# Kernel optimization log

Measured on AMD Instinct MI355X. Metric: run time of the kernel, lower is better.

## Reference

```python
import jax, jax.numpy as jnp
import numpy as np

KNN_K = 3
EPS = 1e-8


def _make_poses(key, batch):
    """Random valid SE(3) matrices [B,4,4] (rotation via QR, small translation)."""
    k1, k2 = jax.random.split(key)
    A = jax.random.normal(k1, (batch, 3, 3), dtype=jnp.float32)
    Q, _ = jnp.linalg.qr(A)
    det = jnp.linalg.det(Q)[:, None, None]
    Q = Q * jnp.where(det < 0, -1.0, 1.0)  # ensure proper rotation
    t = jax.random.normal(k2, (batch, 3), dtype=jnp.float32) * 0.5
    pose = jnp.tile(jnp.eye(4, dtype=jnp.float32), (batch, 1, 1))
    pose = pose.at[:, :3, :3].set(Q)
    pose = pose.at[:, :3, 3].set(t)
    return pose


def setup_inputs() -> dict:
    key = jax.random.key(0)
    kq, kr, kf, kp0, kp1 = jax.random.split(key, 5)
    B, N, M = 2, 8192, 8192
    pc0 = jax.random.normal(kq, (B, N, 3), dtype=jnp.float32) * 20.0
    pc1 = jax.random.normal(kr, (B, M, 3), dtype=jnp.float32) * 20.0
    flow1 = jax.random.normal(kf, (B, M, 3), dtype=jnp.float32)
    pose0 = _make_poses(kp0, B)
    pose1 = _make_poses(kp1, B)
    return {"pc0": pc0, "pc1": pc1, "flow1": flow1, "pose0": pose0, "pose1": pose1}


def reference(pc0, pc1, flow1, pose0, pose1):
    # cal_pose0to1: transform from pc0 ego frame into pc1 ego frame
    pose_0to1 = jnp.linalg.inv(pose1) @ pose0            # [B,4,4]
    R = pose_0to1[:, :3, :3]                             # [B,3,3]
    t = pose_0to1[:, :3, 3]                              # [B,3]
    # pc0_in_pc1 = pc0 @ R^T + t
    pc0_t = jnp.einsum("bij,bnj->bni", R, pc0) + t[:, None, :]  # [B,N,3]
    pose_flow = pc0_t - pc0                              # ego-motion displacement

    # pairwise squared distances (cdist^2) via GEMM form: [B,N,M]
    q2 = jnp.sum(pc0_t * pc0_t, axis=-1)                 # [B,N]
    r2 = jnp.sum(pc1 * pc1, axis=-1)                     # [B,M]
    cross = jnp.einsum("bnd,bmd->bnm", pc0_t, pc1)
    d2 = q2[:, :, None] + r2[:, None, :] - 2.0 * cross

    # KNN: k smallest distances
    neg_d2, idx = jax.lax.top_k(-d2, KNN_K)              # [B,N,k]
    d = jnp.sqrt(jnp.maximum(-neg_d2, 0.0))

    # inverse-distance weights over the k neighbors
    w = 1.0 / (d + EPS)
    w = w / jnp.sum(w, axis=-1, keepdims=True)           # [B,N,k]

    # gather neighbor flows: flow1 [B,M,3] -> [B,N,k,3]
    gathered = jnp.take_along_axis(flow1[:, None, :, :], idx[..., None], axis=2)
    flow_interp = jnp.sum(w[..., None] * gathered, axis=2)  # [B,N,3]
    return flow_interp, pose_flow
```

## Files before the change

### kernel.cpp

```cpp
#include <hip/hip_runtime.h>
#include <math.h>
#include <float.h>
#include <limits.h>

#define CS   64
#define CT   32
#define TILE_PTS (CT * CS)
#define CSP  65
#define QB1  64
#define QT   16
#define MARGIN 0.05f
typedef unsigned long long ull;
typedef float v2f __attribute__((ext_vector_type(2)));
#define KMAX 0xFFFFFFFFFFFFFFFFull

__device__ __forceinline__ unsigned int ford(float f) {
    unsigned int b = __float_as_uint(f);
    return b ^ (((unsigned int)((int)b >> 31)) | 0x80000000u);
}
__device__ __forceinline__ float funord(unsigned int u) {
    unsigned int m = ((u >> 31) - 1u) | 0x80000000u;
    return __uint_as_float(u ^ m);
}

__device__ __forceinline__ ull umin64(ull a, ull b) { return a < b ? a : b; }
__device__ __forceinline__ ull umax64(ull a, ull b) { return a > b ? a : b; }

__device__ __forceinline__ void ins3k(ull k, ull& k0, ull& k1, ull& k2) {
    ull n2 = umax64(k1, umin64(k2, k));
    ull n1 = umax64(k0, umin64(k1, k));
    k0 = umin64(k0, k);
    k1 = n1;
    k2 = n2;
}

__device__ __forceinline__ void sins(float d, float& a0, float& a1, float& a2)
{
    float n1 = __builtin_amdgcn_fmed3f(a0, a1, d);
    float n2 = __builtin_amdgcn_fmed3f(a1, a2, d);
    a0 = fminf(a0, d);
    a1 = n1;
    a2 = n2;
}

__device__ __forceinline__ void pose_rel(const float* __restrict__ P0,
                                         const float* __restrict__ P1,
                                         float R[3][3], float tv[3])
{
    float dt0 = P0[3]  - P1[3];
    float dt1 = P0[7]  - P1[7];
    float dt2 = P0[11] - P1[11];
    #pragma unroll
    for (int i = 0; i < 3; ++i) {
        float a0 = P1[i], a1 = P1[4 + i], a2 = P1[8 + i];
        #pragma unroll
        for (int j = 0; j < 3; ++j)
            R[i][j] = fmaf(a2, P0[8 + j], fmaf(a1, P0[4 + j], a0 * P0[j]));
        tv[i] = fmaf(a2, dt2, fmaf(a1, dt1, a0 * dt0));
    }
}

__launch_bounds__(256, 3)
__global__ void knn_phaseA(const float* __restrict__ pc0,
                           const float* __restrict__ pc1,
                           const float* __restrict__ pose0,
                           const float* __restrict__ pose1,
                           float* __restrict__ cmin,
                           int B, int N, int M, int cstride)
{
    __shared__ float4 tile[CT * CSP];
    __shared__ float4 qd[QB1];

    const int tid = threadIdx.x;
    const int b   = blockIdx.z;
    const int ctb = blockIdx.y;
    const int qb  = blockIdx.x * QB1;
    const int pbase = ctb * TILE_PTS;

    if (tid < QB1) {
        float R[3][3], tv[3];
        pose_rel(pose0 + b * 16, pose1 + b * 16, R, tv);
        int qg0 = qb + tid;
        int qg  = (qg0 < N) ? qg0 : (N - 1);
        const float px = pc0[(size_t)(b * N + qg) * 3 + 0];
        const float py = pc0[(size_t)(b * N + qg) * 3 + 1];
        const float pz = pc0[(size_t)(b * N + qg) * 3 + 2];
        float qx = fmaf(R[0][2], pz, fmaf(R[0][1], py, R[0][0] * px)) + tv[0];
        float qy = fmaf(R[1][2], pz, fmaf(R[1][1], py, R[1][0] * px)) + tv[1];
        float qz = fmaf(R[2][2], pz, fmaf(R[2][1], py, R[2][0] * px)) + tv[2];
        qd[tid] = make_float4(qx, qy, qz,
                              (qx * qx + qy * qy) + qz * qz);
    }

    #pragma unroll
    for (int k = 0; k < TILE_PTS / (256 * 4); ++k) {
        const int pl = (tid + k * 256) * 4;
        const int p  = pbase + pl;
        const int c  = pl >> 6;
        const int off = pl & (CS - 1);
        float4* dst = &tile[c * CSP + off];
        float x0,y0,z0, x1,y1,z1, x2,y2,z2, x3,y3,z3;
        if (p + 3 < M) {
            const float4* pf = (const float4*)(pc1 + (size_t)(b * M + p) * 3);
            float4 A = pf[0], Bv = pf[1], C = pf[2];
            x0 = A.x;  y0 = A.y;  z0 = A.z;
            x1 = A.w;  y1 = Bv.x; z1 = Bv.y;
            x2 = Bv.z; y2 = Bv.w; z2 = C.x;
            x3 = C.y;  y3 = C.z;  z3 = C.w;
        } else {
            float tx[4], ty[4], tz[4];
            #pragma unroll
            for (int u = 0; u < 4; ++u) {
                int pp = p + u;
                if (pp < M) {
                    const float* s = pc1 + (size_t)(b * M + pp) * 3;
                    tx[u] = s[0]; ty[u] = s[1]; tz[u] = s[2];
                } else {
                    tx[u] = 0.f; ty[u] = 0.f; tz[u] = 0.f;
                }
            }
            x0 = tx[0]; y0 = ty[0]; z0 = tz[0];
            x1 = tx[1]; y1 = ty[1]; z1 = tz[1];
            x2 = tx[2]; y2 = ty[2]; z2 = tz[2];
            x3 = tx[3]; y3 = ty[3]; z3 = tz[3];
        }
        float r0 = (p + 0 < M) ? (x0 * x0 + y0 * y0) + z0 * z0 : FLT_MAX;
        float r1 = (p + 1 < M) ? (x1 * x1 + y1 * y1) + z1 * z1 : FLT_MAX;
        float r2 = (p + 2 < M) ? (x2 * x2 + y2 * y2) + z2 * z2 : FLT_MAX;
        float r3 = (p + 3 < M) ? (x3 * x3 + y3 * y3) + z3 * z3 : FLT_MAX;
        dst[0] = make_float4(-2.f * x0, -2.f * x1, -2.f * y0, -2.f * y1);
        dst[1] = make_float4(-2.f * z0, -2.f * z1, r0, r1);
        dst[2] = make_float4(-2.f * x2, -2.f * x3, -2.f * y2, -2.f * y3);
        dst[3] = make_float4(-2.f * z2, -2.f * z3, r2, r3);
    }
    __syncthreads();

    const int w    = tid >> 6;
    const int lane = tid & 63;
    const int cl   = lane & 31;
    const int part = lane >> 5;

    v2f qx2[QT], qy2[QT], qz2[QT];
    #pragma unroll
    for (int t = 0; t < QT; ++t) {
        float4 qq = qd[w * QT + t];
        qx2[t] = (v2f)(qq.x);
        qy2[t] = (v2f)(qq.y);
        qz2[t] = (v2f)(qq.z);
    }

    float mm[QT];
    #pragma unroll
    for (int t = 0; t < QT; ++t) mm[t] = FLT_MAX;

    const float4* tp = &tile[cl * CSP + part * 32];
    #pragma unroll 2
    for (int i2 = 0; i2 < 16; ++i2) {
        const float4 xy = tp[2 * i2];
        const float4 zw = tp[2 * i2 + 1];
        v2f X = {xy.x, xy.y};
        v2f Y = {xy.z, xy.w};
        v2f Z = {zw.x, zw.y};
        v2f W = {zw.z, zw.w};
        #pragma unroll
        for (int t = 0; t < QT; ++t) {
            v2f kk;
            asm("v_pk_fma_f32 %0, %1, %2, %3"
                : "=v"(kk) : "v"(Z), "v"(qz2[t]), "v"(W));
            asm("v_pk_fma_f32 %0, %1, %2, %0"
                : "+v"(kk) : "v"(Y), "v"(qy2[t]));
            asm("v_pk_fma_f32 %0, %1, %2, %0"
                : "+v"(kk) : "v"(X), "v"(qx2[t]));
            mm[t] = fminf(mm[t], fminf(kk.x, kk.y));
        }
    }

    #pragma unroll
    for (int t = 0; t < QT; ++t)
        mm[t] = fminf(mm[t], __shfl_xor(mm[t], 32));

    if (part == 0) {
        const int cg = ctb * CT + cl;
        #pragma unroll
        for (int t = 0; t < QT; ++t) {
            int qg0 = qb + w * QT + t;
            int qg  = (qg0 < N) ? qg0 : (N - 1);
            cmin[((size_t)b * N + qg) * cstride + cg] = mm[t];
        }
    }
}

__launch_bounds__(256, 8)
__global__ void knn_select(const float* __restrict__ pc0,
                           const float* __restrict__ pc1,
                           const float* __restrict__ flow1,
                           const float* __restrict__ pose0,
                           const float* __restrict__ pose1,
                           const float* __restrict__ cmin,
                           float* __restrict__ out,
                           int B, int N, int M, int cstride)
{
    const int tid  = threadIdx.x;
    const int w    = tid >> 6;
    const int lane = tid & 63;
    const int g    = lane >> 4;
    const int l    = lane & 15;

    const int bx = blockIdx.x;
    int qbi, sub;
    if ((gridDim.x & 31) == 0) {
        qbi = (bx & 7) + 8 * (bx >> 5);
        sub = (bx >> 3) & 3;
    } else {
        qbi = bx >> 2;
        sub = bx & 3;
    }

    const int b    = blockIdx.y;
    const int q0   = qbi * QB1 + sub * 16 + w * 4 + g;
    const bool qvalid = (q0 < N);
    const int q    = qvalid ? q0 : (N - 1);

    const size_t row = (size_t)(b * N + q) * cstride;
    const float4 sA = *(const float4*)&cmin[row + l * 8];
    const float4 sB = *(const float4*)&cmin[row + l * 8 + 4];

    float R[3][3], tv[3];
    pose_rel(pose0 + b * 16, pose1 + b * 16, R, tv);
    const float px = pc0[(size_t)(b * N + q) * 3 + 0];
    const float py = pc0[(size_t)(b * N + q) * 3 + 1];
    const float pz = pc0[(size_t)(b * N + q) * 3 + 2];
    const float qx = fmaf(R[0][2], pz, fmaf(R[0][1], py, R[0][0] * px)) + tv[0];
    const float qy = fmaf(R[1][2], pz, fmaf(R[1][1], py, R[1][0] * px)) + tv[1];
    const float qz = fmaf(R[2][2], pz, fmaf(R[2][1], py, R[2][0] * px)) + tv[2];
    const float q2 = (qx * qx + qy * qy) + qz * qz;

    float a0 = FLT_MAX, a1 = FLT_MAX, a2 = FLT_MAX;
    sins(sA.x, a0, a1, a2); sins(sA.y, a0, a1, a2);
    sins(sA.z, a0, a1, a2); sins(sA.w, a0, a1, a2);
    sins(sB.x, a0, a1, a2); sins(sB.y, a0, a1, a2);
    sins(sB.z, a0, a1, a2); sins(sB.w, a0, a1, a2);
    #pragma unroll
    for (int msk = 1; msk <= 8; msk <<= 1) {
        float o0 = __shfl_xor(a0, msk);
        float o1 = __shfl_xor(a1, msk);
        float o2 = __shfl_xor(a2, msk);
        sins(o0, a0, a1, a2);
        sins(o1, a0, a1, a2);
        sins(o2, a0, a1, a2);
    }
    const float thr = a2 + MARGIN;

    unsigned int mbits =
          ((unsigned int)(sA.x <= thr) << 0) | ((unsigned int)(sA.y <= thr) << 1)
        | ((unsigned int)(sA.z <= thr) << 2) | ((unsigned int)(sA.w <= thr) << 3)
        | ((unsigned int)(sB.x <= thr) << 4) | ((unsigned int)(sB.y <= thr) << 5)
        | ((unsigned int)(sB.z <= thr) << 6) | ((unsigned int)(sB.w <= thr) << 7);
    ull m0 = (l < 8) ? ((ull)mbits << (8 * l)) : 0ull;
    ull m1 = (l >= 8) ? ((ull)mbits << (8 * (l - 8))) : 0ull;
    #pragma unroll
    for (int msk = 1; msk <= 8; msk <<= 1) {
        m0 |= __shfl_xor(m0, msk);
        m1 |= __shfl_xor(m1, msk);
    }

    ull kA0 = KMAX, kA1 = KMAX, kA2 = KMAX;
    ull kB0 = KMAX, kB1 = KMAX, kB2 = KMAX;
    #pragma unroll
    for (int half = 0; half < 2; ++half) {
        ull mask = half ? m1 : m0;
        const int cbase = half * 64;
        while (mask) {
            const int ck = (int)__builtin_ctzll(mask);
            mask &= mask - 1;
            const int mb = (cbase + ck) * CS;
            #pragma unroll
            for (int r = 0; r < CS / 16; ++r) {
                const int m = mb + r * 16 + l;
                if (m < M) {
                    const float* pp = pc1 + (size_t)(b * M + m) * 3;
                    float x = pp[0], y = pp[1], z = pp[2];
                    float r2 = (x * x + y * y) + z * z;
                    float cr = fmaf(qz, z, fmaf(qy, y, qx * x));
                    float dd = fmaf(-2.0f, cr, q2 + r2);
                    ull kk = ((ull)ford(dd) << 32) | (unsigned int)m;
                    if (r & 1) ins3k(kk, kB0, kB1, kB2);
                    else       ins3k(kk, kA0, kA1, kA2);
                }
            }
        }
    }
    ins3k(kB0, kA0, kA1, kA2);
    ins3k(kB1, kA0, kA1, kA2);
    ins3k(kB2, kA0, kA1, kA2);

    #pragma unroll
    for (int msk = 1; msk <= 8; msk <<= 1) {
        ull o0 = __shfl_xor(kA0, msk);
        ull o1 = __shfl_xor(kA1, msk);
        ull o2 = __shfl_xor(kA2, msk);
        ins3k(o0, kA0, kA1, kA2);
        ins3k(o1, kA0, kA1, kA2);
        ins3k(o2, kA0, kA1, kA2);
    }

    if (l == 0 && qvalid) {
        size_t pf = (size_t)B * N * 3 + (size_t)(b * N + q) * 3;
        out[pf + 0] = qx - px;
        out[pf + 1] = qy - py;
        out[pf + 2] = qz - pz;

        float D0 = funord((unsigned int)(kA0 >> 32));
        float D1 = funord((unsigned int)(kA1 >> 32));
        float D2 = funord((unsigned int)(kA2 >> 32));
        int   i0 = (int)(unsigned int)kA0;
        int   i1 = (int)(unsigned int)kA1;
        int   i2 = (int)(unsigned int)kA2;

        float dd0 = sqrtf(fmaxf(D0, 0.f));
        float dd1 = sqrtf(fmaxf(D1, 0.f));
        float dd2 = sqrtf(fmaxf(D2, 0.f));
        float w0 = 1.0f / (dd0 + 1e-8f);
        float w1 = 1.0f / (dd1 + 1e-8f);
        float w2 = 1.0f / (dd2 + 1e-8f);
        float wsum = (w0 + w1) + w2;
        w0 /= wsum; w1 /= wsum; w2 /= wsum;

        const float* f0 = flow1 + (size_t)(b * M + i0) * 3;
        const float* f1 = flow1 + (size_t)(b * M + i1) * 3;
        const float* f2 = flow1 + (size_t)(b * M + i2) * 3;

        const size_t ob = (size_t)(b * N + q) * 3;
        #pragma unroll
        for (int c = 0; c < 3; ++c) {
            float p0 = w0 * f0[c];
            float p1 = w1 * f1[c];
            float p2 = w2 * f2[c];
            out[ob + c] = (p0 + p1) + p2;
        }
    }
}

extern "C" void kernel_launch(void* const* d_in, const int* in_sizes, int n_in,
                              void* d_out, int out_size, void* d_ws, size_t ws_size,
                              hipStream_t stream) {
    const float* pc0   = (const float*)d_in[0];
    const float* pc1   = (const float*)d_in[1];
    const float* flow1 = (const float*)d_in[2];
    const float* pose0 = (const float*)d_in[3];
    const float* pose1 = (const float*)d_in[4];
    float* out = (float*)d_out;

    const int B = in_sizes[3] / 16;
    const int N = in_sizes[0] / (3 * B);
    const int M = in_sizes[1] / (3 * B);

    const int nct     = (M + TILE_PTS - 1) / TILE_PTS;
    const int cstride = nct * CT;

    float* cmin = (float*)d_ws;

    dim3 g1((N + QB1 - 1) / QB1, nct, B);
    knn_phaseA<<<g1, dim3(256), 0, stream>>>(pc0, pc1, pose0, pose1,
                                             cmin, B, N, M, cstride);

    dim3 g2((N + 15) / 16, B);
    knn_select<<<g2, dim3(256), 0, stream>>>(pc0, pc1, flow1, pose0, pose1,
                                             cmin, out, B, N, M, cstride);
}
```

Before: 35.66 us.

## Fuse chunk-min distance pass and KNN selection into one kernel

Merges the two-kernel KNN pipeline into a single kernel. Each 512-thread block scans all reference points for its 64 queries in two LDS-tiled passes and keeps the per-chunk minima in shared memory instead of global workspace. It then runs the threshold-and-rescan selection and the flow interpolation in place. This removes the global cmin write and read and one kernel launch, but the grid shrinks to one block per query group, which lowers parallelism. The pass count and cmin stride are hardcoded to cover M up to 8192.

```diff
diff --git a/kernel.cpp b/kernel.cpp
--- a/kernel.cpp
+++ b/kernel.cpp
@@ -3,12 +3,14 @@
 #include <float.h>
 #include <limits.h>
 
-#define CS   64
-#define CT   32
-#define TILE_PTS (CT * CS)
-#define CSP  65
-#define QB1  64
-#define QT   16
+#define CS    64
+#define CTP   64
+#define PASS_PTS (CTP * CS)
+#define CSP   65
+#define QPB   64
+#define QT    8
+#define NPASS 2
+#define CMSTRIDE 132
 #define MARGIN 0.05f
 typedef unsigned long long ull;
 typedef float v2f __attribute__((ext_vector_type(2)));
@@ -60,85 +62,46 @@
     }
 }
 
-__launch_bounds__(256, 3)
-__global__ void knn_phaseA(const float* __restrict__ pc0,
-                           const float* __restrict__ pc1,
-                           const float* __restrict__ pose0,
-                           const float* __restrict__ pose1,
-                           float* __restrict__ cmin,
-                           int B, int N, int M, int cstride)
+__launch_bounds__(512, 2)
+__global__ void knn_fused(const float* __restrict__ pc0,
+                          const float* __restrict__ pc1,
+                          const float* __restrict__ flow1,
+                          const float* __restrict__ pose0,
+                          const float* __restrict__ pose1,
+                          float* __restrict__ out,
+                          int B, int N, int M)
 {
-    __shared__ float4 tile[CT * CSP];
-    __shared__ float4 qd[QB1];
+    __shared__ float4 tile[CTP * CSP];
+    __shared__ float4 qd[QPB];
 
     const int tid = threadIdx.x;
-    const int b   = blockIdx.z;
-    const int ctb = blockIdx.y;
-    const int qb  = blockIdx.x * QB1;
-    const int pbase = ctb * TILE_PTS;
-
-    if (tid < QB1) {
+    const int b   = blockIdx.y;
+    const int qb  = blockIdx.x * QPB;
+
+    if (tid < QPB) {
         float R[3][3], tv[3];
         pose_rel(pose0 + b * 16, pose1 + b * 16, R, tv);
         int qg0 = qb + tid;
-        int qg  = (qg0 < N) ? qg0 : (N - 1);
+        bool valid = qg0 < N;
+        int qg = valid ? qg0 : (N - 1);
         const float px = pc0[(size_t)(b * N + qg) * 3 + 0];
         const float py = pc0[(size_t)(b * N + qg) * 3 + 1];
         const float pz = pc0[(size_t)(b * N + qg) * 3 + 2];
         float qx = fmaf(R[0][2], pz, fmaf(R[0][1], py, R[0][0] * px)) + tv[0];
         float qy = fmaf(R[1][2], pz, fmaf(R[1][1], py, R[1][0] * px)) + tv[1];
         float qz = fmaf(R[2][2], pz, fmaf(R[2][1], py, R[2][0] * px)) + tv[2];
-        qd[tid] = make_float4(qx, qy, qz,
-                              (qx * qx + qy * qy) + qz * qz);
-    }
-
-    #pragma unroll
-    for (int k = 0; k < TILE_PTS / (256 * 4); ++k) {
-        const int pl = (tid + k * 256) * 4;
-        const int p  = pbase + pl;
-        const int c  = pl >> 6;
-        const int off = pl & (CS - 1);
-        float4* dst = &tile[c * CSP + off];
-        float x0,y0,z0, x1,y1,z1, x2,y2,z2, x3,y3,z3;
-        if (p + 3 < M) {
-            const float4* pf = (const float4*)(pc1 + (size_t)(b * M + p) * 3);
-            float4 A = pf[0], Bv = pf[1], C = pf[2];
-            x0 = A.x;  y0 = A.y;  z0 = A.z;
-            x1 = A.w;  y1 = Bv.x; z1 = Bv.y;
-            x2 = Bv.z; y2 = Bv.w; z2 = C.x;
-            x3 = C.y;  y3 = C.z;  z3 = C.w;
-        } else {
-            float tx[4], ty[4], tz[4];
-            #pragma unroll
-            for (int u = 0; u < 4; ++u) {
-                int pp = p + u;
-                if (pp < M) {
-                    const float* s = pc1 + (size_t)(b * M + pp) * 3;
-                    tx[u] = s[0]; ty[u] = s[1]; tz[u] = s[2];
-                } else {
-                    tx[u] = 0.f; ty[u] = 0.f; tz[u] = 0.f;
-                }
-            }
-            x0 = tx[0]; y0 = ty[0]; z0 = tz[0];
-            x1 = tx[1]; y1 = ty[1]; z1 = tz[1];
-            x2 = tx[2]; y2 = ty[2]; z2 = tz[2];
-            x3 = tx[3]; y3 = ty[3]; z3 = tz[3];
-        }
-        float r0 = (p + 0 < M) ? (x0 * x0 + y0 * y0) + z0 * z0 : FLT_MAX;
-        float r1 = (p + 1 < M) ? (x1 * x1 + y1 * y1) + z1 * z1 : FLT_MAX;
-        float r2 = (p + 2 < M) ? (x2 * x2 + y2 * y2) + z2 * z2 : FLT_MAX;
-        float r3 = (p + 3 < M) ? (x3 * x3 + y3 * y3) + z3 * z3 : FLT_MAX;
-        dst[0] = make_float4(-2.f * x0, -2.f * x1, -2.f * y0, -2.f * y1);
-        dst[1] = make_float4(-2.f * z0, -2.f * z1, r0, r1);
-        dst[2] = make_float4(-2.f * x2, -2.f * x3, -2.f * y2, -2.f * y3);
-        dst[3] = make_float4(-2.f * z2, -2.f * z3, r2, r3);
+        qd[tid] = make_float4(qx, qy, qz, (qx * qx + qy * qy) + qz * qz);
+        if (valid) {
+            size_t pf = (size_t)B * N * 3 + (size_t)(b * N + qg) * 3;
+            out[pf + 0] = qx - px;
+            out[pf + 1] = qy - py;
+            out[pf + 2] = qz - pz;
+        }
     }
     __syncthreads();
 
     const int w    = tid >> 6;
     const int lane = tid & 63;
-    const int cl   = lane & 31;
-    const int part = lane >> 5;
 
     v2f qx2[QT], qy2[QT], qz2[QT];
     #pragma unroll
@@ -149,194 +112,204 @@
         qz2[t] = (v2f)(qq.z);
     }
 
-    float mm[QT];
+    float mm[NPASS][QT];
     #pragma unroll
-    for (int t = 0; t < QT; ++t) mm[t] = FLT_MAX;
-
-    const float4* tp = &tile[cl * CSP + part * 32];
-    #pragma unroll 2
-    for (int i2 = 0; i2 < 16; ++i2) {
-        const float4 xy = tp[2 * i2];
-        const float4 zw = tp[2 * i2 + 1];
-        v2f X = {xy.x, xy.y};
-        v2f Y = {xy.z, xy.w};
-        v2f Z = {zw.x, zw.y};
-        v2f W = {zw.z, zw.w};
-        #pragma unroll
-        for (int t = 0; t < QT; ++t) {
-            v2f kk;
-            asm("v_pk_fma_f32 %0, %1, %2, %3"
-                : "=v"(kk) : "v"(Z), "v"(qz2[t]), "v"(W));
-            asm("v_pk_fma_f32 %0, %1, %2, %0"
-                : "+v"(kk) : "v"(Y), "v"(qy2[t]));
-            asm("v_pk_fma_f32 %0, %1, %2, %0"
-                : "+v"(kk) : "v"(X), "v"(qx2[t]));
-            mm[t] = fminf(mm[t], fminf(kk.x, kk.y));
-        }
-    }
-
+    for (int pp = 0; pp < NPASS; ++pp)
+        #pragma unroll
+        for (int t = 0; t < QT; ++t) mm[pp][t] = FLT_MAX;
+
+    for (int pass = 0; pass < NPASS; ++pass) {
+        if (pass) __syncthreads();
+
+        #pragma unroll
+        for (int k = 0; k < PASS_PTS / (512 * 4); ++k) {
+            const int pl = (tid + k * 512) * 4;
+            const int p  = pass * PASS_PTS + pl;
+            const int c  = pl >> 6;
+            const int off = pl & (CS - 1);
+            float4* dst = &tile[c * CSP + off];
+            float x0,y0,z0, x1,y1,z1, x2,y2,z2, x3,y3,z3;
+            if (p + 3 < M) {
+                const float4* pf = (const float4*)(pc1 + (size_t)(b * M + p) * 3);
+                float4 A = pf[0], Bv = pf[1], C = pf[2];
+                x0 = A.x;  y0 = A.y;  z0 = A.z;
+                x1 = A.w;  y1 = Bv.x; z1 = Bv.y;
+                x2 = Bv.z; y2 = Bv.w; z2 = C.x;
+                x3 = C.y;  y3 = C.z;  z3 = C.w;
+            } else {
+                float tx[4], ty[4], tz[4];
+                #pragma unroll
+                for (int u = 0; u < 4; ++u) {
+                    int pp2 = p + u;
+                    if (pp2 < M) {
+                        const float* s = pc1 + (size_t)(b * M + pp2) * 3;
+                        tx[u] = s[0]; ty[u] = s[1]; tz[u] = s[2];
+                    } else {
+                        tx[u] = 0.f; ty[u] = 0.f; tz[u] = 0.f;
+                    }
+                }
+                x0 = tx[0]; y0 = ty[0]; z0 = tz[0];
+                x1 = tx[1]; y1 = ty[1]; z1 = tz[1];
+                x2 = tx[2]; y2 = ty[2]; z2 = tz[2];
+                x3 = tx[3]; y3 = ty[3]; z3 = tz[3];
+            }
+            float r0 = (p + 0 < M) ? (x0 * x0 + y0 * y0) + z0 * z0 : FLT_MAX;
+            float r1 = (p + 1 < M) ? (x1 * x1 + y1 * y1) + z1 * z1 : FLT_MAX;
+            float r2 = (p + 2 < M) ? (x2 * x2 + y2 * y2) + z2 * z2 : FLT_MAX;
+            float r3 = (p + 3 < M) ? (x3 * x3 + y3 * y3) + z3 * z3 : FLT_MAX;
+            dst[0] = make_float4(-2.f * x0, -2.f * x1, -2.f * y0, -2.f * y1);
+            dst[1] = make_float4(-2.f * z0, -2.f * z1, r0, r1);
+            dst[2] = make_float4(-2.f * x2, -2.f * x3, -2.f * y2, -2.f * y3);
+            dst[3] = make_float4(-2.f * z2, -2.f * z3, r2, r3);
+        }
+        __syncthreads();
+
+        const float4* tp = &tile[lane * CSP];
+        #pragma unroll 4
+        for (int i = 0; i < 32; ++i) {
+            const float4 xy = tp[2 * i];
+            const float4 zw = tp[2 * i + 1];
+            v2f X = {xy.x, xy.y};
+            v2f Y = {xy.z, xy.w};
+            v2f Z = {zw.x, zw.y};
+            v2f W = {zw.z, zw.w};
+            #pragma unroll
+            for (int t = 0; t < QT; ++t) {
+                v2f kk;
+                asm("v_pk_fma_f32 %0, %1, %2, %3"
+                    : "=v"(kk) : "v"(Z), "v"(qz2[t]), "v"(W));
+                asm("v_pk_fma_f32 %0, %1, %2, %0"
+                    : "+v"(kk) : "v"(Y), "v"(qy2[t]));
+                asm("v_pk_fma_f32 %0, %1, %2, %0"
+                    : "+v"(kk) : "v"(X), "v"(qx2[t]));
+                mm[pass][t] = fminf(mm[pass][t], fminf(kk.x, kk.y));
+            }
+        }
+    }
+
+    __syncthreads();
+
+    float* cminL = (float*)tile;
     #pragma unroll
-    for (int t = 0; t < QT; ++t)
-        mm[t] = fminf(mm[t], __shfl_xor(mm[t], 32));
-
-    if (part == 0) {
-        const int cg = ctb * CT + cl;
-        #pragma unroll
-        for (int t = 0; t < QT; ++t) {
-            int qg0 = qb + w * QT + t;
-            int qg  = (qg0 < N) ? qg0 : (N - 1);
-            cmin[((size_t)b * N + qg) * cstride + cg] = mm[t];
-        }
-    }
-}
-
-__launch_bounds__(256, 8)
-__global__ void knn_select(const float* __restrict__ pc0,
-                           const float* __restrict__ pc1,
-                           const float* __restrict__ flow1,
-                           const float* __restrict__ pose0,
-                           const float* __restrict__ pose1,
-                           const float* __restrict__ cmin,
-                           float* __restrict__ out,
-                           int B, int N, int M, int cstride)
-{
-    const int tid  = threadIdx.x;
-    const int w    = tid >> 6;
-    const int lane = tid & 63;
-    const int g    = lane >> 4;
-    const int l    = lane & 15;
-
-    const int bx = blockIdx.x;
-    int qbi, sub;
-    if ((gridDim.x & 31) == 0) {
-        qbi = (bx & 7) + 8 * (bx >> 5);
-        sub = (bx >> 3) & 3;
-    } else {
-        qbi = bx >> 2;
-        sub = bx & 3;
-    }
-
-    const int b    = blockIdx.y;
-    const int q0   = qbi * QB1 + sub * 16 + w * 4 + g;
-    const bool qvalid = (q0 < N);
-    const int q    = qvalid ? q0 : (N - 1);
-
-    const size_t row = (size_t)(b * N + q) * cstride;
-    const float4 sA = *(const float4*)&cmin[row + l * 8];
-    const float4 sB = *(const float4*)&cmin[row + l * 8 + 4];
-
-    float R[3][3], tv[3];
-    pose_rel(pose0 + b * 16, pose1 + b * 16, R, tv);
-    const float px = pc0[(size_t)(b * N + q) * 3 + 0];
-    const float py = pc0[(size_t)(b * N + q) * 3 + 1];
-    const float pz = pc0[(size_t)(b * N + q) * 3 + 2];
-    const float qx = fmaf(R[0][2], pz, fmaf(R[0][1], py, R[0][0] * px)) + tv[0];
-    const float qy = fmaf(R[1][2], pz, fmaf(R[1][1], py, R[1][0] * px)) + tv[1];
-    const float qz = fmaf(R[2][2], pz, fmaf(R[2][1], py, R[2][0] * px)) + tv[2];
-    const float q2 = (qx * qx + qy * qy) + qz * qz;
-
-    float a0 = FLT_MAX, a1 = FLT_MAX, a2 = FLT_MAX;
-    sins(sA.x, a0, a1, a2); sins(sA.y, a0, a1, a2);
-    sins(sA.z, a0, a1, a2); sins(sA.w, a0, a1, a2);
-    sins(sB.x, a0, a1, a2); sins(sB.y, a0, a1, a2);
-    sins(sB.z, a0, a1, a2); sins(sB.w, a0, a1, a2);
-    #pragma unroll
-    for (int msk = 1; msk <= 8; msk <<= 1) {
-        float o0 = __shfl_xor(a0, msk);
-        float o1 = __shfl_xor(a1, msk);
-        float o2 = __shfl_xor(a2, msk);
-        sins(o0, a0, a1, a2);
-        sins(o1, a0, a1, a2);
-        sins(o2, a0, a1, a2);
-    }
-    const float thr = a2 + MARGIN;
-
-    unsigned int mbits =
-          ((unsigned int)(sA.x <= thr) << 0) | ((unsigned int)(sA.y <= thr) << 1)
-        | ((unsigned int)(sA.z <= thr) << 2) | ((unsigned int)(sA.w <= thr) << 3)
-        | ((unsigned int)(sB.x <= thr) << 4) | ((unsigned int)(sB.y <= thr) << 5)
-        | ((unsigned int)(sB.z <= thr) << 6) | ((unsigned int)(sB.w <= thr) << 7);
-    ull m0 = (l < 8) ? ((ull)mbits << (8 * l)) : 0ull;
-    ull m1 = (l >= 8) ? ((ull)mbits << (8 * (l - 8))) : 0ull;
-    #pragma unroll
-    for (int msk = 1; msk <= 8; msk <<= 1) {
-        m0 |= __shfl_xor(m0, msk);
-        m1 |= __shfl_xor(m1, msk);
-    }
-
-    ull kA0 = KMAX, kA1 = KMAX, kA2 = KMAX;
-    ull kB0 = KMAX, kB1 = KMAX, kB2 = KMAX;
-    #pragma unroll
-    for (int half = 0; half < 2; ++half) {
-        ull mask = half ? m1 : m0;
-        const int cbase = half * 64;
-        while (mask) {
-            const int ck = (int)__builtin_ctzll(mask);
-            mask &= mask - 1;
-            const int mb = (cbase + ck) * CS;
-            #pragma unroll
-            for (int r = 0; r < CS / 16; ++r) {
-                const int m = mb + r * 16 + l;
-                if (m < M) {
-                    const float* pp = pc1 + (size_t)(b * M + m) * 3;
-                    float x = pp[0], y = pp[1], z = pp[2];
-                    float r2 = (x * x + y * y) + z * z;
-                    float cr = fmaf(qz, z, fmaf(qy, y, qx * x));
-                    float dd = fmaf(-2.0f, cr, q2 + r2);
-                    ull kk = ((ull)ford(dd) << 32) | (unsigned int)m;
-                    if (r & 1) ins3k(kk, kB0, kB1, kB2);
-                    else       ins3k(kk, kA0, kA1, kA2);
+    for (int t = 0; t < QT; ++t) {
+        const int ql = w * QT + t;
+        cminL[ql * CMSTRIDE + lane]       = mm[0][t];
+        cminL[ql * CMSTRIDE + CTP + lane] = mm[1][t];
+    }
+    __syncthreads();
+
+    const int g = tid >> 4;
+    const int l = tid & 15;
+
+    for (int round = 0; round < QPB / 32; ++round) {
+        const int ql = round * 32 + g;
+        const int q0 = qb + ql;
+        const bool qvalid = (q0 < N);
+        const int q = qvalid ? q0 : (N - 1);
+
+        const float4 sA = *(const float4*)&cminL[ql * CMSTRIDE + l * 8];
+        const float4 sB = *(const float4*)&cminL[ql * CMSTRIDE + l * 8 + 4];
+        const float4 qq = qd[ql];
+        const float qx = qq.x, qy = qq.y, qz = qq.z, q2 = qq.w;
+
+        float a0 = FLT_MAX, a1 = FLT_MAX, a2 = FLT_MAX;
+        sins(sA.x, a0, a1, a2); sins(sA.y, a0, a1, a2);
+        sins(sA.z, a0, a1, a2); sins(sA.w, a0, a1, a2);
+        sins(sB.x, a0, a1, a2); sins(sB.y, a0, a1, a2);
+        sins(sB.z, a0, a1, a2); sins(sB.w, a0, a1, a2);
+        #pragma unroll
+        for (int msk = 1; msk <= 8; msk <<= 1) {
+            float o0 = __shfl_xor(a0, msk);
+            float o1 = __shfl_xor(a1, msk);
+            float o2 = __shfl_xor(a2, msk);
+            sins(o0, a0, a1, a2);
+            sins(o1, a0, a1, a2);
+            sins(o2, a0, a1, a2);
+        }
+        const float thr = a2 + MARGIN;
+
+        unsigned int mbits =
+              ((unsigned int)(sA.x <= thr) << 0) | ((unsigned int)(sA.y <= thr) << 1)
+            | ((unsigned int)(sA.z <= thr) << 2) | ((unsigned int)(sA.w <= thr) << 3)
+            | ((unsigned int)(sB.x <= thr) << 4) | ((unsigned int)(sB.y <= thr) << 5)
+            | ((unsigned int)(sB.z <= thr) << 6) | ((unsigned int)(sB.w <= thr) << 7);
+        ull m0 = (l < 8) ? ((ull)mbits << (8 * l)) : 0ull;
+        ull m1 = (l >= 8) ? ((ull)mbits << (8 * (l - 8))) : 0ull;
+        #pragma unroll
+        for (int msk = 1; msk <= 8; msk <<= 1) {
+            m0 |= __shfl_xor(m0, msk);
+            m1 |= __shfl_xor(m1, msk);
+        }
+
+        ull kA0 = KMAX, kA1 = KMAX, kA2 = KMAX;
+        ull kB0 = KMAX, kB1 = KMAX, kB2 = KMAX;
+        #pragma unroll
+        for (int half = 0; half < 2; ++half) {
+            ull mask = half ? m1 : m0;
+            const int cbase = half * 64;
+            while (mask) {
+                const int ck = (int)__builtin_ctzll(mask);
+                mask &= mask - 1;
+                const int mb = (cbase + ck) * CS;
+                #pragma unroll
+                for (int r = 0; r < CS / 16; ++r) {
+                    const int m = mb + r * 16 + l;
+                    if (m < M) {
+                        const float* pp = pc1 + (size_t)(b * M + m) * 3;
+                        float x = pp[0], y = pp[1], z = pp[2];
+                        float r2 = (x * x + y * y) + z * z;
+                        float cr = fmaf(qz, z, fmaf(qy, y, qx * x));
+                        float dd = fmaf(-2.0f, cr, q2 + r2);
+                        ull kk = ((ull)ford(dd) << 32) | (unsigned int)m;
+                        if (r & 1) ins3k(kk, kB0, kB1, kB2);
+                        else       ins3k(kk, kA0, kA1, kA2);
+                    }
                 }
             }
         }
-    }
-    ins3k(kB0, kA0, kA1, kA2);
-    ins3k(kB1, kA0, kA1, kA2);
-    ins3k(kB2, kA0, kA1, kA2);
-
-    #pragma unroll
-    for (int msk = 1; msk <= 8; msk <<= 1) {
-        ull o0 = __shfl_xor(kA0, msk);
-        ull o1 = __shfl_xor(kA1, msk);
-        ull o2 = __shfl_xor(kA2, msk);
-        ins3k(o0, kA0, kA1, kA2);
-        ins3k(o1, kA0, kA1, kA2);
-        ins3k(o2, kA0, kA1, kA2);
-    }
-
-    if (l == 0 && qvalid) {
-        size_t pf = (size_t)B * N * 3 + (size_t)(b * N + q) * 3;
-        out[pf + 0] = qx - px;
-        out[pf + 1] = qy - py;
-        out[pf + 2] = qz - pz;
-
-        float D0 = funord((unsigned int)(kA0 >> 32));
-        float D1 = funord((unsigned int)(kA1 >> 32));
-        float D2 = funord((unsigned int)(kA2 >> 32));
-        int   i0 = (int)(unsigned int)kA0;
-        int   i1 = (int)(unsigned int)kA1;
-        int   i2 = (int)(unsigned int)kA2;
-
-        float dd0 = sqrtf(fmaxf(D0, 0.f));
-        float dd1 = sqrtf(fmaxf(D1, 0.f));
-        float dd2 = sqrtf(fmaxf(D2, 0.f));
-        float w0 = 1.0f / (dd0 + 1e-8f);
-        float w1 = 1.0f / (dd1 + 1e-8f);
-        float w2 = 1.0f / (dd2 + 1e-8f);
-        float wsum = (w0 + w1) + w2;
-        w0 /= wsum; w1 /= wsum; w2 /= wsum;
-
-        const float* f0 = flow1 + (size_t)(b * M + i0) * 3;
-        const float* f1 = flow1 + (size_t)(b * M + i1) * 3;
-        const float* f2 = flow1 + (size_t)(b * M + i2) * 3;
-
-        const size_t ob = (size_t)(b * N + q) * 3;
-        #pragma unroll
-        for (int c = 0; c < 3; ++c) {
-            float p0 = w0 * f0[c];
-            float p1 = w1 * f1[c];
-            float p2 = w2 * f2[c];
-            out[ob + c] = (p0 + p1) + p2;
+        ins3k(kB0, kA0, kA1, kA2);
+        ins3k(kB1, kA0, kA1, kA2);
+        ins3k(kB2, kA0, kA1, kA2);
+
+        #pragma unroll
+        for (int msk = 1; msk <= 8; msk <<= 1) {
+            ull o0 = __shfl_xor(kA0, msk);
+            ull o1 = __shfl_xor(kA1, msk);
+            ull o2 = __shfl_xor(kA2, msk);
+            ins3k(o0, kA0, kA1, kA2);
+            ins3k(o1, kA0, kA1, kA2);
+            ins3k(o2, kA0, kA1, kA2);
+        }
+
+        if (l == 0 && qvalid) {
+            float D0 = funord((unsigned int)(kA0 >> 32));
+            float D1 = funord((unsigned int)(kA1 >> 32));
+            float D2 = funord((unsigned int)(kA2 >> 32));
+            int   i0 = (int)(unsigned int)kA0;
+            int   i1 = (int)(unsigned int)kA1;
+            int   i2 = (int)(unsigned int)kA2;
+
+            float dd0 = sqrtf(fmaxf(D0, 0.f));
+            float dd1 = sqrtf(fmaxf(D1, 0.f));
+            float dd2 = sqrtf(fmaxf(D2, 0.f));
+            float w0 = 1.0f / (dd0 + 1e-8f);
+            float w1 = 1.0f / (dd1 + 1e-8f);
+            float w2 = 1.0f / (dd2 + 1e-8f);
+            float wsum = (w0 + w1) + w2;
+            w0 /= wsum; w1 /= wsum; w2 /= wsum;
+
+            const float* f0 = flow1 + (size_t)(b * M + i0) * 3;
+            const float* f1 = flow1 + (size_t)(b * M + i1) * 3;
+            const float* f2 = flow1 + (size_t)(b * M + i2) * 3;
+
+            const size_t ob = (size_t)(b * N + q) * 3;
+            #pragma unroll
+            for (int c = 0; c < 3; ++c) {
+                float p0 = w0 * f0[c];
+                float p1 = w1 * f1[c];
+                float p2 = w2 * f2[c];
+                out[ob + c] = (p0 + p1) + p2;
+            }
         }
     }
 }
@@ -355,16 +328,7 @@
     const int N = in_sizes[0] / (3 * B);
     const int M = in_sizes[1] / (3 * B);
 
-    const int nct     = (M + TILE_PTS - 1) / TILE_PTS;
-    const int cstride = nct * CT;
-
-    float* cmin = (float*)d_ws;
-
-    dim3 g1((N + QB1 - 1) / QB1, nct, B);
-    knn_phaseA<<<g1, dim3(256), 0, stream>>>(pc0, pc1, pose0, pose1,
-                                             cmin, B, N, M, cstride);
-
-    dim3 g2((N + 15) / 16, B);
-    knn_select<<<g2, dim3(256), 0, stream>>>(pc0, pc1, flow1, pose0, pose1,
-                                             cmin, out, B, N, M, cstride);
-}
+    dim3 grid((N + QPB - 1) / QPB, B);
+    knn_fused<<<grid, dim3(512), 0, stream>>>(pc0, pc1, flow1, pose0, pose1,
+                                              out, B, N, M);
+}
```

Measured after the change: 37.48 us. +5.1%, slower.
